# Kernel tuning notes

Measured on AMD Instinct MI355X. Metric: run time of the kernel, lower is better.

Reference implementation:

```python
import jax, jax.numpy as jnp
import numpy as np

N, E, H, C = 50000, 1_600_000, 4, 32
DIN, DE = 128, 32
NEG_SLOPE = 0.2  # PyG GATConv leaky_relu negative_slope default


def setup_inputs() -> dict:
    key = jax.random.key(0)
    ks = jax.random.split(key, 12)
    s = 0.1  # weight scale
    return {
        "x": jax.random.normal(ks[0], (N, DIN), jnp.float32),
        "edge_index": jax.random.randint(ks[1], (2, E), 0, N, jnp.int32),
        "edge_attr": jax.random.normal(ks[2], (E, DE), jnp.float32),
        "W": jax.random.normal(ks[3], (DIN, H * C), jnp.float32) * s,
        "att_src": jax.random.normal(ks[4], (H, C), jnp.float32) * s,
        "att_dst": jax.random.normal(ks[5], (H, C), jnp.float32) * s,
        "lin_edge_W": jax.random.normal(ks[6], (DE, H * C), jnp.float32) * s,
        "att_edge": jax.random.normal(ks[7], (H, C), jnp.float32) * s,
        "bias": jax.random.normal(ks[8], (H * C,), jnp.float32) * s,
        "proj_W": jax.random.normal(ks[9], (H * C, C), jnp.float32) * s,
        "proj_b": jax.random.normal(ks[10], (C,), jnp.float32) * s,
    }


def reference(x, edge_index, edge_attr, W, att_src, att_dst, lin_edge_W,
              att_edge, bias, proj_W, proj_b):
    n = x.shape[0]
    h, c = att_src.shape
    src, dst = edge_index[0], edge_index[1]

    # add self loops; loop edge_attr = mean of incoming edge_attr (PyG fill_value='mean')
    deg = jax.ops.segment_sum(jnp.ones(src.shape, x.dtype), dst, num_segments=n)
    ea_mean = jax.ops.segment_sum(edge_attr, dst, num_segments=n) / jnp.maximum(deg, 1.0)[:, None]
    loop = jnp.arange(n, dtype=src.dtype)
    src = jnp.concatenate([src, loop])
    dst = jnp.concatenate([dst, loop])
    ea = jnp.concatenate([edge_attr, ea_mean], axis=0)

    xl = (x @ W).reshape(n, h, c)                       # [N,H,C]
    a_src = jnp.einsum('nhc,hc->nh', xl, att_src)       # [N,H]
    a_dst = jnp.einsum('nhc,hc->nh', xl, att_dst)
    e = (ea @ lin_edge_W).reshape(-1, h, c)             # [E',H,C]
    a_e = jnp.einsum('ehc,hc->eh', e, att_edge)

    alpha = jax.nn.leaky_relu(a_src[src] + a_dst[dst] + a_e, NEG_SLOPE)  # [E',H]
    amax = jax.lax.stop_gradient(jax.ops.segment_max(alpha, dst, num_segments=n))
    alpha = jnp.exp(alpha - amax[dst])
    denom = jax.ops.segment_sum(alpha, dst, num_segments=n)
    alpha = alpha / (denom[dst] + 1e-16)                # segment softmax over incoming edges

    out = jax.ops.segment_sum(xl[src] * alpha[..., None], dst, num_segments=n)  # [N,H,C]
    out = out.reshape(n, h * c) + bias                  # concat heads + bias
    return out @ proj_W + proj_b                        # concat projection
```

## Files before the change

### kernel.cpp

```cpp
#include <hip/hip_runtime.h>

#define NEG_SLOPE 0.2f

__device__ __forceinline__ float lrelu(float x) { return x > 0.0f ? x : NEG_SLOPE * x; }

__device__ __forceinline__ float bcast(float v, int srcLane) {
  return __int_as_float(__builtin_amdgcn_readlane(__float_as_int(v), srcLane));
}

__device__ __forceinline__ unsigned pack_bf16(float a, float b) {
  unsigned ua = __float_as_uint(a), ub = __float_as_uint(b);
  ua += 0x7fffu + ((ua >> 16) & 1u);
  ub += 0x7fffu + ((ub >> 16) & 1u);
  return (ua >> 16) | (ub & 0xffff0000u);
}
__device__ __forceinline__ float bf16lo(unsigned z) { return __uint_as_float(z << 16); }
__device__ __forceinline__ float bf16hi(unsigned z) { return __uint_as_float(z & 0xffff0000u); }

__global__ void k0_setup(const float* __restrict__ W, const float* __restrict__ proj_W,
                         const float* __restrict__ att_src, const float* __restrict__ att_dst,
                         const float* __restrict__ lin_edge_W, const float* __restrict__ att_edge,
                         const float* __restrict__ bias, const float* __restrict__ proj_b,
                         float* __restrict__ Wz, float* __restrict__ Ws, float* __restrict__ Wd,
                         float* __restrict__ M, float* __restrict__ cproj) {
  int t = blockIdx.x * blockDim.x + threadIdx.x;
  if (t < 16384) {
    int d = t >> 7, o = t & 127;
    int h = o >> 5, jj = o & 31;
    float s = 0.f;
    #pragma unroll
    for (int c = 0; c < 32; ++c)
      s += W[d * 128 + h * 32 + c] * proj_W[(h * 32 + c) * 32 + jj];
    Wz[d * 128 + o] = s;
  } else if (t < 16384 + 512) {
    int idx = t - 16384; int d = idx >> 2, h = idx & 3;
    float s = 0.f;
    #pragma unroll
    for (int c = 0; c < 32; ++c) s += W[d * 128 + h * 32 + c] * att_src[h * 32 + c];
    Ws[d * 4 + h] = s;
  } else if (t < 16384 + 1024) {
    int idx = t - 16384 - 512; int d = idx >> 2, h = idx & 3;
    float s = 0.f;
    #pragma unroll
    for (int c = 0; c < 32; ++c) s += W[d * 128 + h * 32 + c] * att_dst[h * 32 + c];
    Wd[d * 4 + h] = s;
  } else if (t < 16384 + 1024 + 128) {
    int idx = t - 16384 - 1024; int d = idx >> 2, h = idx & 3;
    float s = 0.f;
    #pragma unroll
    for (int c = 0; c < 32; ++c) s += lin_edge_W[d * 128 + h * 32 + c] * att_edge[h * 32 + c];
    M[d * 4 + h] = s;
  } else if (t < 16384 + 1024 + 128 + 32) {
    int jj = t - 16384 - 1024 - 128;
    float s = proj_b[jj];
    #pragma unroll
    for (int k = 0; k < 128; ++k) s += bias[k] * proj_W[k * 32 + jj];
    cproj[jj] = s;
  }
}

__global__ __launch_bounds__(256) void k3_gemm(
    const float* __restrict__ x, const float* __restrict__ Wz,
    const float* __restrict__ Ws, const float* __restrict__ Wd,
    int n, unsigned* __restrict__ Zp, float* __restrict__ a_src, float* __restrict__ a_dst) {
  __shared__ float2 Wl[128 * 64];
  int tid = threadIdx.x;
  for (int idx = tid; idx < 128 * 64; idx += 256) {
    int k = idx >> 6, l = idx & 63;
    Wl[idx] = make_float2(Wz[k * 128 + l], Wz[k * 128 + 64 + l]);
  }
  __syncthreads();
  int lane = tid & 63, wid = tid >> 6;
  float ws0[4], ws1[4], wd0[4], wd1[4];
  #pragma unroll
  for (int h = 0; h < 4; ++h) {
    ws0[h] = Ws[lane * 4 + h];  ws1[h] = Ws[(64 + lane) * 4 + h];
    wd0[h] = Wd[lane * 4 + h];  wd1[h] = Wd[(64 + lane) * 4 + h];
  }
  int gw = blockIdx.x * 4 + wid;
  int nw = gridDim.x * 4;
  for (int base = gw * 4; base < n; base += nw * 4) {
    float xa[4], xb[4];
    #pragma unroll
    for (int u = 0; u < 4; ++u) {
      int node = base + u;
      xa[u] = (node < n) ? x[node * 128 + lane] : 0.0f;
      xb[u] = (node < n) ? x[node * 128 + 64 + lane] : 0.0f;
    }
    float acc0[4] = {0.f, 0.f, 0.f, 0.f}, acc1[4] = {0.f, 0.f, 0.f, 0.f};
    #pragma unroll 16
    for (int k = 0; k < 64; ++k) {
      float2 w = Wl[k * 64 + lane];
      #pragma unroll
      for (int u = 0; u < 4; ++u) {
        float xv = bcast(xa[u], k);
        acc0[u] += xv * w.x; acc1[u] += xv * w.y;
      }
    }
    #pragma unroll 16
    for (int k = 0; k < 64; ++k) {
      float2 w = Wl[(64 + k) * 64 + lane];
      #pragma unroll
      for (int u = 0; u < 4; ++u) {
        float xv = bcast(xb[u], k);
        acc0[u] += xv * w.x; acc1[u] += xv * w.y;
      }
    }
    #pragma unroll
    for (int u = 0; u < 4; ++u) {
      int node = base + u;
      if (node >= n) break;
      Zp[(size_t)node * 64 + lane] = pack_bf16(acc0[u], acc1[u]);
      float ps[4], pd[4];
      #pragma unroll
      for (int h = 0; h < 4; ++h) {
        ps[h] = xa[u] * ws0[h] + xb[u] * ws1[h];
        pd[h] = xa[u] * wd0[h] + xb[u] * wd1[h];
      }
      #pragma unroll
      for (int m = 1; m < 64; m <<= 1) {
        #pragma unroll
        for (int h = 0; h < 4; ++h) {
          ps[h] += __shfl_xor(ps[h], m);
          pd[h] += __shfl_xor(pd[h], m);
        }
      }
      if (lane == 0) {
        *(float4*)&a_src[node * 4] = make_float4(ps[0], ps[1], ps[2], ps[3]);
        *(float4*)&a_dst[node * 4] = make_float4(pd[0], pd[1], pd[2], pd[3]);
      }
    }
  }
}

__global__ __launch_bounds__(256) void k1_edge(
    const int* __restrict__ ei, int E, const float4* __restrict__ ea4,
    const float* __restrict__ Mg,
    const float* __restrict__ a_src, const float* __restrict__ a_dst,
    uint4* __restrict__ we, int* __restrict__ deg, int* __restrict__ rank) {
  __shared__ float4 s_ea[256 * 9];
  __shared__ float4 Msh[32];
  int t = threadIdx.x;
  if (t < 32) Msh[t] = ((const float4*)Mg)[t];
  int B0 = blockIdx.x * 256;
  #pragma unroll
  for (int k = 0; k < 8; ++k) {
    int f = k * 256 + t;
    int e = B0 + (f >> 3);
    float4 v = (e < E) ? ea4[(size_t)B0 * 8 + f] : make_float4(0.f, 0.f, 0.f, 0.f);
    s_ea[(f >> 3) * 9 + (f & 7)] = v;
  }
  __syncthreads();
  int e = B0 + t;
  if (e >= E) return;
  int s = ei[e], d = ei[E + e];
  float4 as = *(const float4*)&a_src[(size_t)s * 4];
  float4 ad = *(const float4*)&a_dst[(size_t)d * 4];
  float ae0 = 0.f, ae1 = 0.f, ae2 = 0.f, ae3 = 0.f;
  #pragma unroll
  for (int j = 0; j < 8; ++j) {
    float4 v = s_ea[t * 9 + j];
    float4 m0 = Msh[j * 4 + 0], m1 = Msh[j * 4 + 1], m2 = Msh[j * 4 + 2], m3 = Msh[j * 4 + 3];
    ae0 += v.x * m0.x + v.y * m1.x + v.z * m2.x + v.w * m3.x;
    ae1 += v.x * m0.y + v.y * m1.y + v.z * m2.y + v.w * m3.y;
    ae2 += v.x * m0.z + v.y * m1.z + v.z * m2.z + v.w * m3.z;
    ae3 += v.x * m0.w + v.y * m1.w + v.z * m2.w + v.w * m3.w;
  }
  float w0 = __expf(lrelu(ae0 + as.x + ad.x));
  float w1 = __expf(lrelu(ae1 + as.y + ad.y));
  float w2 = __expf(lrelu(ae2 + as.z + ad.z));
  float w3 = __expf(lrelu(ae3 + as.w + ad.w));
  we[e] = make_uint4(pack_bf16(w0, w1), pack_bf16(w2, w3),
                     pack_bf16(ae0, ae1), pack_bf16(ae2, ae3));
  rank[e] = atomicAdd(&deg[d], 1);
}

__global__ void k2_scan(const int* __restrict__ deg, int n, int* __restrict__ offsets) {
  __shared__ int shw[16];
  __shared__ int shtot;
  int tid = threadIdx.x;
  int lane = tid & 63, wid = tid >> 6;
  int running = 0;
  for (int base = 0; base < n; base += 4096) {
    int i = base + tid * 4;
    int4 v = make_int4(0, 0, 0, 0);
    if (i + 3 < n) v = *(const int4*)&deg[i];
    else {
      if (i < n) v.x = deg[i];
      if (i + 1 < n) v.y = deg[i + 1];
      if (i + 2 < n) v.z = deg[i + 2];
      if (i + 3 < n) v.w = deg[i + 3];
    }
    int tsum = v.x + v.y + v.z + v.w;
    int inc = tsum;
    #pragma unroll
    for (int s = 1; s < 64; s <<= 1) {
      int t = __shfl_up(inc, s);
      if (lane >= s) inc += t;
    }
    if (lane == 63) shw[wid] = inc;
    __syncthreads();
    if (wid == 0) {
      int w = (lane < 16) ? shw[lane] : 0;
      int winc = w;
      #pragma unroll
      for (int s = 1; s < 16; s <<= 1) {
        int t = __shfl_up(winc, s);
        if (lane >= s) winc += t;
      }
      if (lane < 16) shw[lane] = winc - w;
      if (lane == 15) shtot = winc;
    }
    __syncthreads();
    int excl = running + shw[wid] + inc - tsum;
    if (i < n)     offsets[i + 1] = excl + v.x;
    if (i + 1 < n) offsets[i + 2] = excl + v.x + v.y;
    if (i + 2 < n) offsets[i + 3] = excl + v.x + v.y + v.z;
    if (i + 3 < n) offsets[i + 4] = excl + tsum;
    running += shtot;
    __syncthreads();
  }
  if (tid == 0) offsets[0] = 0;
}

__global__ void k4_scatter(const int* __restrict__ ei, int E,
                           const int* __restrict__ rank, const int* __restrict__ offsets,
                           const uint4* __restrict__ we, uint4* __restrict__ csr) {
  int e = blockIdx.x * blockDim.x + threadIdx.x;
  if (e >= E) return;
  int s = ei[e], d = ei[E + e];
  int slot = offsets[d] + rank[e];
  uint4 w = we[e];
  uint4* ent = &csr[(size_t)slot * 2];
  *(int*)ent = s;
  ent[1] = w;
}

__global__ __launch_bounds__(256) void k5_agg(
    const int* __restrict__ offsets, const uint4* __restrict__ csr,
    const unsigned* __restrict__ Zp,
    const float* __restrict__ a_src, const float* __restrict__ a_dst,
    const float* __restrict__ cproj, int n, float* __restrict__ out) {
  __shared__ float4 s_w[4][64];
  __shared__ int    s_s[4][64];
  int tid = threadIdx.x;
  int lane = tid & 63, wid = tid >> 6;
  int gw = blockIdx.x * 4 + wid, nw = gridDim.x * 4;
  int h0 = lane >> 5, j = lane & 31;
  float cp = cproj[j];
  const float* wbase = (const float*)&s_w[wid][0];
  for (int node = gw; node < n; node += nw) {
    int off0 = offsets[node], off1 = offsets[node + 1];
    int dg = off1 - off0;
    float dsx = 0.f, dsy = 0.f, dsz = 0.f, dsw = 0.f;
    float aex = 0.f, aey = 0.f, aez = 0.f, aew = 0.f;
    float agg0 = 0.f, agg1 = 0.f;
    for (int base = off0; base < off1; base += 64) {
      int rem = off1 - base; if (rem > 64) rem = 64;
      if (lane < rem) {
        const uint4* ent = &csr[(size_t)(base + lane) * 2];
        int s = *(const int*)ent;
        uint4 w = ent[1];
        float w0 = bf16lo(w.x), w1 = bf16hi(w.x);
        float w2 = bf16lo(w.y), w3 = bf16hi(w.y);
        dsx += w0; dsy += w1; dsz += w2; dsw += w3;
        aex += bf16lo(w.z); aey += bf16hi(w.z);
        aez += bf16lo(w.w); aew += bf16hi(w.w);
        s_w[wid][lane] = make_float4(w0, w2, w1, w3);
        s_s[wid][lane] = s;
      }
      int jj = 0;
      for (; jj + 4 <= rem; jj += 4) {
        int s0 = s_s[wid][jj], s1 = s_s[wid][jj + 1];
        int s2 = s_s[wid][jj + 2], s3 = s_s[wid][jj + 3];
        unsigned z0 = Zp[(size_t)s0 * 64 + lane];
        unsigned z1 = Zp[(size_t)s1 * 64 + lane];
        unsigned z2 = Zp[(size_t)s2 * 64 + lane];
        unsigned z3 = Zp[(size_t)s3 * 64 + lane];
        float2 w0 = *(const float2*)(wbase + (jj    ) * 4 + 2 * h0);
        float2 w1 = *(const float2*)(wbase + (jj + 1) * 4 + 2 * h0);
        float2 w2 = *(const float2*)(wbase + (jj + 2) * 4 + 2 * h0);
        float2 w3 = *(const float2*)(wbase + (jj + 3) * 4 + 2 * h0);
        agg0 += w0.x * bf16lo(z0) + w1.x * bf16lo(z1) + w2.x * bf16lo(z2) + w3.x * bf16lo(z3);
        agg1 += w0.y * bf16hi(z0) + w1.y * bf16hi(z1) + w2.y * bf16hi(z2) + w3.y * bf16hi(z3);
      }
      for (; jj < rem; ++jj) {
        int s0 = s_s[wid][jj];
        unsigned z0 = Zp[(size_t)s0 * 64 + lane];
        float2 w0 = *(const float2*)(wbase + jj * 4 + 2 * h0);
        agg0 += w0.x * bf16lo(z0);
        agg1 += w0.y * bf16hi(z0);
      }
    }
    #pragma unroll
    for (int m = 1; m < 64; m <<= 1) {
      dsx += __shfl_xor(dsx, m); dsy += __shfl_xor(dsy, m);
      dsz += __shfl_xor(dsz, m); dsw += __shfl_xor(dsw, m);
      aex += __shfl_xor(aex, m); aey += __shfl_xor(aey, m);
      aez += __shfl_xor(aez, m); aew += __shfl_xor(aew, m);
    }
    float invd = 1.0f / (float)(dg > 0 ? dg : 1);
    float4 asn = *(const float4*)&a_src[node * 4];
    float4 ad  = *(const float4*)&a_dst[node * 4];
    float w0 = __expf(lrelu(asn.x + ad.x + aex * invd));
    float w1 = __expf(lrelu(asn.y + ad.y + aey * invd));
    float w2 = __expf(lrelu(asn.z + ad.z + aez * invd));
    float w3 = __expf(lrelu(asn.w + ad.w + aew * invd));
    dsx += w0; dsy += w1; dsz += w2; dsw += w3;
    unsigned zpn = Zp[(size_t)node * 64 + lane];
    float sw0 = h0 ? w1 : w0, sw1 = h0 ? w3 : w2;
    agg0 += sw0 * bf16lo(zpn);
    agg1 += sw1 * bf16hi(zpn);
    float d0 = h0 ? dsy : dsx, d1 = h0 ? dsw : dsz;
    float tt = agg0 / (d0 + 1e-16f) + agg1 / (d1 + 1e-16f);
    tt += __shfl_xor(tt, 32);
    if (lane < 32) out[node * 32 + j] = tt + cp;
  }
}

extern "C" void kernel_launch(void* const* d_in, const int* in_sizes, int n_in,
                              void* d_out, int out_size, void* d_ws, size_t ws_size,
                              hipStream_t stream) {
  const float* x          = (const float*)d_in[0];
  const int*   ei         = (const int*)  d_in[1];
  const float* ea         = (const float*)d_in[2];
  const float* W          = (const float*)d_in[3];
  const float* att_src    = (const float*)d_in[4];
  const float* att_dst    = (const float*)d_in[5];
  const float* lin_edge_W = (const float*)d_in[6];
  const float* att_edge   = (const float*)d_in[7];
  const float* bias       = (const float*)d_in[8];
  const float* proj_W     = (const float*)d_in[9];
  const float* proj_b     = (const float*)d_in[10];
  float* out = (float*)d_out;
  int N = in_sizes[0] / 128;
  int E = in_sizes[1] / 2;

  char* p = (char*)d_ws;
  auto alloc = [&](size_t bytes) {
    char* r = p;
    p += (bytes + 255) & ~(size_t)255;
    return r;
  };
  unsigned* Zp     = (unsigned*)alloc((size_t)N * 64 * 4);
  float* a_src     = (float*)alloc((size_t)N * 4 * 4);
  float* a_dst     = (float*)alloc((size_t)N * 4 * 4);
  int*   deg       = (int*)  alloc((size_t)N * 4);
  int*   offsets   = (int*)  alloc((size_t)(N + 1) * 4);
  int*   rank      = (int*)  alloc((size_t)E * 4);
  uint4* we        = (uint4*)alloc((size_t)E * 16);
  uint4* csr       = (uint4*)alloc((size_t)E * 32);
  float* Wz        = (float*)alloc(128 * 128 * 4);
  float* Ws        = (float*)alloc(128 * 4 * 4);
  float* Wd        = (float*)alloc(128 * 4 * 4);
  float* M         = (float*)alloc(32 * 4 * 4);
  float* cproj     = (float*)alloc(32 * 4);

  hipMemsetAsync(deg, 0, (size_t)N * 4, stream);

  k0_setup<<<69, 256, 0, stream>>>(W, proj_W, att_src, att_dst, lin_edge_W, att_edge,
                                   bias, proj_b, Wz, Ws, Wd, M, cproj);
  k3_gemm<<<512, 256, 0, stream>>>(x, Wz, Ws, Wd, N, Zp, a_src, a_dst);
  k1_edge<<<(E + 255) / 256, 256, 0, stream>>>(ei, E, (const float4*)ea, M,
                                               a_src, a_dst, we, deg, rank);
  k2_scan<<<1, 1024, 0, stream>>>(deg, N, offsets);
  k4_scatter<<<(E + 255) / 256, 256, 0, stream>>>(ei, E, rank, offsets, we, csr);
  k5_agg<<<2048, 256, 0, stream>>>(offsets, csr, Zp, a_src, a_dst, cproj, N, out);
}
```

Baseline: 558.9 us.

## Build CSR directly in edge kernel and compute softmax weights during aggregation

A separate degree-count kernel and a scan now run first, so the edge kernel can claim CSR slots with an atomic on a per-node cursor and write 16-byte entries (source index plus bf16 edge logits) straight into the CSR. This removes the rank and we intermediate arrays and the separate scatter kernel, and halves the CSR entry size. Exponentiated attention weights are now computed in the aggregation kernel from a_src gathers, which adds a random gather and four exps per edge there. Edge order within a node becomes nondeterministic, so float summation order can vary between runs.

```diff
diff --git a/kernel.cpp b/kernel.cpp
--- a/kernel.cpp
+++ b/kernel.cpp
@@ -133,49 +133,23 @@
   }
 }
 
-__global__ __launch_bounds__(256) void k1_edge(
-    const int* __restrict__ ei, int E, const float4* __restrict__ ea4,
-    const float* __restrict__ Mg,
-    const float* __restrict__ a_src, const float* __restrict__ a_dst,
-    uint4* __restrict__ we, int* __restrict__ deg, int* __restrict__ rank) {
-  __shared__ float4 s_ea[256 * 9];
-  __shared__ float4 Msh[32];
-  int t = threadIdx.x;
-  if (t < 32) Msh[t] = ((const float4*)Mg)[t];
-  int B0 = blockIdx.x * 256;
-  #pragma unroll
-  for (int k = 0; k < 8; ++k) {
-    int f = k * 256 + t;
-    int e = B0 + (f >> 3);
-    float4 v = (e < E) ? ea4[(size_t)B0 * 8 + f] : make_float4(0.f, 0.f, 0.f, 0.f);
-    s_ea[(f >> 3) * 9 + (f & 7)] = v;
-  }
-  __syncthreads();
-  int e = B0 + t;
-  if (e >= E) return;
-  int s = ei[e], d = ei[E + e];
-  float4 as = *(const float4*)&a_src[(size_t)s * 4];
-  float4 ad = *(const float4*)&a_dst[(size_t)d * 4];
-  float ae0 = 0.f, ae1 = 0.f, ae2 = 0.f, ae3 = 0.f;
-  #pragma unroll
-  for (int j = 0; j < 8; ++j) {
-    float4 v = s_ea[t * 9 + j];
-    float4 m0 = Msh[j * 4 + 0], m1 = Msh[j * 4 + 1], m2 = Msh[j * 4 + 2], m3 = Msh[j * 4 + 3];
-    ae0 += v.x * m0.x + v.y * m1.x + v.z * m2.x + v.w * m3.x;
-    ae1 += v.x * m0.y + v.y * m1.y + v.z * m2.y + v.w * m3.y;
-    ae2 += v.x * m0.z + v.y * m1.z + v.z * m2.z + v.w * m3.z;
-    ae3 += v.x * m0.w + v.y * m1.w + v.z * m2.w + v.w * m3.w;
-  }
-  float w0 = __expf(lrelu(ae0 + as.x + ad.x));
-  float w1 = __expf(lrelu(ae1 + as.y + ad.y));
-  float w2 = __expf(lrelu(ae2 + as.z + ad.z));
-  float w3 = __expf(lrelu(ae3 + as.w + ad.w));
-  we[e] = make_uint4(pack_bf16(w0, w1), pack_bf16(w2, w3),
-                     pack_bf16(ae0, ae1), pack_bf16(ae2, ae3));
-  rank[e] = atomicAdd(&deg[d], 1);
-}
-
-__global__ void k2_scan(const int* __restrict__ deg, int n, int* __restrict__ offsets) {
+__global__ __launch_bounds__(256) void kA_deg(const int* __restrict__ ei, int E,
+                                              int* __restrict__ deg) {
+  int t = blockIdx.x * blockDim.x + threadIdx.x;
+  int i = t * 4;
+  if (((E & 3) == 0) && (i + 3 < E)) {
+    int4 d = *(const int4*)&ei[E + i];
+    atomicAdd(&deg[d.x], 1);
+    atomicAdd(&deg[d.y], 1);
+    atomicAdd(&deg[d.z], 1);
+    atomicAdd(&deg[d.w], 1);
+  } else {
+    for (int k = i; k < E && k < i + 4; ++k) atomicAdd(&deg[ei[E + k]], 1);
+  }
+}
+
+__global__ void k2_scan(const int* __restrict__ deg, int n, int* __restrict__ offsets,
+                        int* __restrict__ cnt) {
   __shared__ int shw[16];
   __shared__ int shtot;
   int tid = threadIdx.x;
@@ -213,27 +187,55 @@
     }
     __syncthreads();
     int excl = running + shw[wid] + inc - tsum;
-    if (i < n)     offsets[i + 1] = excl + v.x;
-    if (i + 1 < n) offsets[i + 2] = excl + v.x + v.y;
-    if (i + 2 < n) offsets[i + 3] = excl + v.x + v.y + v.z;
-    if (i + 3 < n) offsets[i + 4] = excl + tsum;
+    if (i + 3 < n) {
+      *(int4*)&offsets[i + 1] = make_int4(excl + v.x, excl + v.x + v.y,
+                                          excl + v.x + v.y + v.z, excl + tsum);
+      *(int4*)&cnt[i] = make_int4(excl, excl + v.x, excl + v.x + v.y,
+                                  excl + v.x + v.y + v.z);
+    } else {
+      if (i < n)     { offsets[i + 1] = excl + v.x;             cnt[i]     = excl; }
+      if (i + 1 < n) { offsets[i + 2] = excl + v.x + v.y;       cnt[i + 1] = excl + v.x; }
+      if (i + 2 < n) { offsets[i + 3] = excl + v.x + v.y + v.z; cnt[i + 2] = excl + v.x + v.y; }
+      if (i + 3 < n) { offsets[i + 4] = excl + tsum;            cnt[i + 3] = excl + v.x + v.y + v.z; }
+    }
     running += shtot;
     __syncthreads();
   }
   if (tid == 0) offsets[0] = 0;
 }
 
-__global__ void k4_scatter(const int* __restrict__ ei, int E,
-                           const int* __restrict__ rank, const int* __restrict__ offsets,
-                           const uint4* __restrict__ we, uint4* __restrict__ csr) {
-  int e = blockIdx.x * blockDim.x + threadIdx.x;
+__global__ __launch_bounds__(256) void k1_edge(
+    const int* __restrict__ ei, int E, const float4* __restrict__ ea4,
+    const float* __restrict__ Mg,
+    int* __restrict__ cnt, uint4* __restrict__ csr) {
+  __shared__ float4 s_ea[256 * 9];
+  __shared__ float4 Msh[32];
+  int t = threadIdx.x;
+  if (t < 32) Msh[t] = ((const float4*)Mg)[t];
+  int B0 = blockIdx.x * 256;
+  #pragma unroll
+  for (int k = 0; k < 8; ++k) {
+    int f = k * 256 + t;
+    int e = B0 + (f >> 3);
+    float4 v = (e < E) ? ea4[(size_t)B0 * 8 + f] : make_float4(0.f, 0.f, 0.f, 0.f);
+    s_ea[(f >> 3) * 9 + (f & 7)] = v;
+  }
+  __syncthreads();
+  int e = B0 + t;
   if (e >= E) return;
   int s = ei[e], d = ei[E + e];
-  int slot = offsets[d] + rank[e];
-  uint4 w = we[e];
-  uint4* ent = &csr[(size_t)slot * 2];
-  *(int*)ent = s;
-  ent[1] = w;
+  int slot = atomicAdd(&cnt[d], 1);
+  float ae0 = 0.f, ae1 = 0.f, ae2 = 0.f, ae3 = 0.f;
+  #pragma unroll
+  for (int j = 0; j < 8; ++j) {
+    float4 v = s_ea[t * 9 + j];
+    float4 m0 = Msh[j * 4 + 0], m1 = Msh[j * 4 + 1], m2 = Msh[j * 4 + 2], m3 = Msh[j * 4 + 3];
+    ae0 += v.x * m0.x + v.y * m1.x + v.z * m2.x + v.w * m3.x;
+    ae1 += v.x * m0.y + v.y * m1.y + v.z * m2.y + v.w * m3.y;
+    ae2 += v.x * m0.z + v.y * m1.z + v.z * m2.z + v.w * m3.z;
+    ae3 += v.x * m0.w + v.y * m1.w + v.z * m2.w + v.w * m3.w;
+  }
+  csr[(size_t)slot] = make_uint4((unsigned)s, pack_bf16(ae0, ae1), pack_bf16(ae2, ae3), 0u);
 }
 
 __global__ __launch_bounds__(256) void k5_agg(
@@ -252,20 +254,24 @@
   for (int node = gw; node < n; node += nw) {
     int off0 = offsets[node], off1 = offsets[node + 1];
     int dg = off1 - off0;
+    float4 ad = *(const float4*)&a_dst[(size_t)node * 4];
     float dsx = 0.f, dsy = 0.f, dsz = 0.f, dsw = 0.f;
     float aex = 0.f, aey = 0.f, aez = 0.f, aew = 0.f;
     float agg0 = 0.f, agg1 = 0.f;
     for (int base = off0; base < off1; base += 64) {
       int rem = off1 - base; if (rem > 64) rem = 64;
       if (lane < rem) {
-        const uint4* ent = &csr[(size_t)(base + lane) * 2];
-        int s = *(const int*)ent;
-        uint4 w = ent[1];
-        float w0 = bf16lo(w.x), w1 = bf16hi(w.x);
-        float w2 = bf16lo(w.y), w3 = bf16hi(w.y);
+        uint4 ent = csr[(size_t)(base + lane)];
+        int s = (int)ent.x;
+        float ae0 = bf16lo(ent.y), ae1 = bf16hi(ent.y);
+        float ae2 = bf16lo(ent.z), ae3 = bf16hi(ent.z);
+        float4 av = *(const float4*)&a_src[(size_t)s * 4];
+        float w0 = __expf(lrelu(ae0 + av.x + ad.x));
+        float w1 = __expf(lrelu(ae1 + av.y + ad.y));
+        float w2 = __expf(lrelu(ae2 + av.z + ad.z));
+        float w3 = __expf(lrelu(ae3 + av.w + ad.w));
         dsx += w0; dsy += w1; dsz += w2; dsw += w3;
-        aex += bf16lo(w.z); aey += bf16hi(w.z);
-        aez += bf16lo(w.w); aew += bf16hi(w.w);
+        aex += ae0; aey += ae1; aez += ae2; aew += ae3;
         s_w[wid][lane] = make_float4(w0, w2, w1, w3);
         s_s[wid][lane] = s;
       }
@@ -300,8 +306,7 @@
       aez += __shfl_xor(aez, m); aew += __shfl_xor(aew, m);
     }
     float invd = 1.0f / (float)(dg > 0 ? dg : 1);
-    float4 asn = *(const float4*)&a_src[node * 4];
-    float4 ad  = *(const float4*)&a_dst[node * 4];
+    float4 asn = *(const float4*)&a_src[(size_t)node * 4];
     float w0 = __expf(lrelu(asn.x + ad.x + aex * invd));
     float w1 = __expf(lrelu(asn.y + ad.y + aey * invd));
     float w2 = __expf(lrelu(asn.z + ad.z + aez * invd));
@@ -346,10 +351,9 @@
   float* a_src     = (float*)alloc((size_t)N * 4 * 4);
   float* a_dst     = (float*)alloc((size_t)N * 4 * 4);
   int*   deg       = (int*)  alloc((size_t)N * 4);
+  int*   cnt       = (int*)  alloc((size_t)N * 4);
   int*   offsets   = (int*)  alloc((size_t)(N + 1) * 4);
-  int*   rank      = (int*)  alloc((size_t)E * 4);
-  uint4* we        = (uint4*)alloc((size_t)E * 16);
-  uint4* csr       = (uint4*)alloc((size_t)E * 32);
+  uint4* csr       = (uint4*)alloc((size_t)E * 16);
   float* Wz        = (float*)alloc(128 * 128 * 4);
   float* Ws        = (float*)alloc(128 * 4 * 4);
   float* Wd        = (float*)alloc(128 * 4 * 4);
@@ -360,10 +364,9 @@
 
   k0_setup<<<69, 256, 0, stream>>>(W, proj_W, att_src, att_dst, lin_edge_W, att_edge,
                                    bias, proj_b, Wz, Ws, Wd, M, cproj);
+  kA_deg<<<(E / 4 + 256) / 256, 256, 0, stream>>>(ei, E, deg);
+  k2_scan<<<1, 1024, 0, stream>>>(deg, N, offsets, cnt);
   k3_gemm<<<512, 256, 0, stream>>>(x, Wz, Ws, Wd, N, Zp, a_src, a_dst);
-  k1_edge<<<(E + 255) / 256, 256, 0, stream>>>(ei, E, (const float4*)ea, M,
-                                               a_src, a_dst, we, deg, rank);
-  k2_scan<<<1, 1024, 0, stream>>>(deg, N, offsets);
-  k4_scatter<<<(E + 255) / 256, 256, 0, stream>>>(ei, E, rank, offsets, we, csr);
+  k1_edge<<<(E + 255) / 256, 256, 0, stream>>>(ei, E, (const float4*)ea, M, cnt, csr);
   k5_agg<<<2048, 256, 0, stream>>>(offsets, csr, Zp, a_src, a_dst, cproj, N, out);
 }
```

New measurement: 595.3 us. 6.5% more time.

## Split degree counting into separate kernel and simplify edge kernel loads

Applied to the files above, without the earlier changes.

Moves the per-destination atomic degree/rank computation out of the edge-attention kernel into its own vectorized kernel that runs before the node GEMM, with the scan moved ahead as well. The edge kernel drops its shared-memory staging of edge attributes and reads each edge's 128-byte row directly. The scatter kernel now writes CSR entries with nontemporal stores and fully writes the padding words. This rearranges the kernel schedule at the cost of reading the edge indices one extra time in a separate pass, and uncoalesced per-thread row reads may hurt bandwidth.

```diff
diff --git a/kernel.cpp b/kernel.cpp
--- a/kernel.cpp
+++ b/kernel.cpp
@@ -1,6 +1,8 @@
 #include <hip/hip_runtime.h>
 
 #define NEG_SLOPE 0.2f
+
+typedef unsigned nuint4 __attribute__((ext_vector_type(4)));
 
 __device__ __forceinline__ float lrelu(float x) { return x > 0.0f ? x : NEG_SLOPE * x; }
 
@@ -133,46 +135,21 @@
   }
 }
 
-__global__ __launch_bounds__(256) void k1_edge(
-    const int* __restrict__ ei, int E, const float4* __restrict__ ea4,
-    const float* __restrict__ Mg,
-    const float* __restrict__ a_src, const float* __restrict__ a_dst,
-    uint4* __restrict__ we, int* __restrict__ deg, int* __restrict__ rank) {
-  __shared__ float4 s_ea[256 * 9];
-  __shared__ float4 Msh[32];
-  int t = threadIdx.x;
-  if (t < 32) Msh[t] = ((const float4*)Mg)[t];
-  int B0 = blockIdx.x * 256;
-  #pragma unroll
-  for (int k = 0; k < 8; ++k) {
-    int f = k * 256 + t;
-    int e = B0 + (f >> 3);
-    float4 v = (e < E) ? ea4[(size_t)B0 * 8 + f] : make_float4(0.f, 0.f, 0.f, 0.f);
-    s_ea[(f >> 3) * 9 + (f & 7)] = v;
-  }
-  __syncthreads();
-  int e = B0 + t;
-  if (e >= E) return;
-  int s = ei[e], d = ei[E + e];
-  float4 as = *(const float4*)&a_src[(size_t)s * 4];
-  float4 ad = *(const float4*)&a_dst[(size_t)d * 4];
-  float ae0 = 0.f, ae1 = 0.f, ae2 = 0.f, ae3 = 0.f;
-  #pragma unroll
-  for (int j = 0; j < 8; ++j) {
-    float4 v = s_ea[t * 9 + j];
-    float4 m0 = Msh[j * 4 + 0], m1 = Msh[j * 4 + 1], m2 = Msh[j * 4 + 2], m3 = Msh[j * 4 + 3];
-    ae0 += v.x * m0.x + v.y * m1.x + v.z * m2.x + v.w * m3.x;
-    ae1 += v.x * m0.y + v.y * m1.y + v.z * m2.y + v.w * m3.y;
-    ae2 += v.x * m0.z + v.y * m1.z + v.z * m2.z + v.w * m3.z;
-    ae3 += v.x * m0.w + v.y * m1.w + v.z * m2.w + v.w * m3.w;
-  }
-  float w0 = __expf(lrelu(ae0 + as.x + ad.x));
-  float w1 = __expf(lrelu(ae1 + as.y + ad.y));
-  float w2 = __expf(lrelu(ae2 + as.z + ad.z));
-  float w3 = __expf(lrelu(ae3 + as.w + ad.w));
-  we[e] = make_uint4(pack_bf16(w0, w1), pack_bf16(w2, w3),
-                     pack_bf16(ae0, ae1), pack_bf16(ae2, ae3));
-  rank[e] = atomicAdd(&deg[d], 1);
+__global__ __launch_bounds__(256) void kA_deg(const int* __restrict__ ei, int E,
+                                              int* __restrict__ deg, int* __restrict__ rank) {
+  int t = blockIdx.x * blockDim.x + threadIdx.x;
+  int i = t * 4;
+  if (((E & 3) == 0) && (i + 3 < E)) {
+    int4 d = *(const int4*)&ei[E + i];
+    int4 r;
+    r.x = atomicAdd(&deg[d.x], 1);
+    r.y = atomicAdd(&deg[d.y], 1);
+    r.z = atomicAdd(&deg[d.z], 1);
+    r.w = atomicAdd(&deg[d.w], 1);
+    *(int4*)&rank[i] = r;
+  } else {
+    for (int k = i; k < E && k < i + 4; ++k) rank[k] = atomicAdd(&deg[ei[E + k]], 1);
+  }
 }
 
 __global__ void k2_scan(const int* __restrict__ deg, int n, int* __restrict__ offsets) {
@@ -223,17 +200,53 @@
   if (tid == 0) offsets[0] = 0;
 }
 
-__global__ void k4_scatter(const int* __restrict__ ei, int E,
+__global__ __launch_bounds__(256) void k1_edge(
+    const int* __restrict__ ei, int E, const float4* __restrict__ ea4,
+    const float* __restrict__ Mg,
+    const float* __restrict__ a_src, const float* __restrict__ a_dst,
+    uint4* __restrict__ we) {
+  __shared__ float4 Msh[32];
+  int t = threadIdx.x;
+  if (t < 32) Msh[t] = ((const float4*)Mg)[t];
+  __syncthreads();
+  int e = blockIdx.x * 256 + t;
+  if (e >= E) return;
+  int s = ei[e], d = ei[E + e];
+  float4 as = *(const float4*)&a_src[(size_t)s * 4];
+  float4 ad = *(const float4*)&a_dst[(size_t)d * 4];
+  const float4* row = ea4 + (size_t)e * 8;
+  float ae0 = 0.f, ae1 = 0.f, ae2 = 0.f, ae3 = 0.f;
+  #pragma unroll
+  for (int j = 0; j < 8; ++j) {
+    float4 v = row[j];
+    float4 m0 = Msh[j * 4 + 0], m1 = Msh[j * 4 + 1], m2 = Msh[j * 4 + 2], m3 = Msh[j * 4 + 3];
+    ae0 += v.x * m0.x + v.y * m1.x + v.z * m2.x + v.w * m3.x;
+    ae1 += v.x * m0.y + v.y * m1.y + v.z * m2.y + v.w * m3.y;
+    ae2 += v.x * m0.z + v.y * m1.z + v.z * m2.z + v.w * m3.z;
+    ae3 += v.x * m0.w + v.y * m1.w + v.z * m2.w + v.w * m3.w;
+  }
+  float w0 = __expf(lrelu(ae0 + as.x + ad.x));
+  float w1 = __expf(lrelu(ae1 + as.y + ad.y));
+  float w2 = __expf(lrelu(ae2 + as.z + ad.z));
+  float w3 = __expf(lrelu(ae3 + as.w + ad.w));
+  we[e] = make_uint4(pack_bf16(w0, w1), pack_bf16(w2, w3),
+                     pack_bf16(ae0, ae1), pack_bf16(ae2, ae3));
+}
+
+__global__ __launch_bounds__(256) void k4_scatter(const int* __restrict__ ei, int E,
                            const int* __restrict__ rank, const int* __restrict__ offsets,
                            const uint4* __restrict__ we, uint4* __restrict__ csr) {
   int e = blockIdx.x * blockDim.x + threadIdx.x;
   if (e >= E) return;
-  int s = ei[e], d = ei[E + e];
+  int d = ei[E + e];
+  int s = ei[e];
   int slot = offsets[d] + rank[e];
   uint4 w = we[e];
-  uint4* ent = &csr[(size_t)slot * 2];
-  *(int*)ent = s;
-  ent[1] = w;
+  nuint4* ent = (nuint4*)&csr[(size_t)slot * 2];
+  nuint4 e0; e0.x = (unsigned)s; e0.y = 0u; e0.z = 0u; e0.w = 0u;
+  nuint4 e1; e1.x = w.x; e1.y = w.y; e1.z = w.z; e1.w = w.w;
+  __builtin_nontemporal_store(e0, ent);
+  __builtin_nontemporal_store(e1, ent + 1);
 }
 
 __global__ __launch_bounds__(256) void k5_agg(
@@ -360,10 +373,11 @@
 
   k0_setup<<<69, 256, 0, stream>>>(W, proj_W, att_src, att_dst, lin_edge_W, att_edge,
                                    bias, proj_b, Wz, Ws, Wd, M, cproj);
+  kA_deg<<<(E / 4 + 255) / 256, 256, 0, stream>>>(ei, E, deg, rank);
+  k2_scan<<<1, 1024, 0, stream>>>(deg, N, offsets);
   k3_gemm<<<512, 256, 0, stream>>>(x, Wz, Ws, Wd, N, Zp, a_src, a_dst);
   k1_edge<<<(E + 255) / 256, 256, 0, stream>>>(ei, E, (const float4*)ea, M,
-                                               a_src, a_dst, we, deg, rank);
-  k2_scan<<<1, 1024, 0, stream>>>(deg, N, offsets);
+                                               a_src, a_dst, we);
   k4_scatter<<<(E + 255) / 256, 256, 0, stream>>>(ei, E, rank, offsets, we, csr);
   k5_agg<<<2048, 256, 0, stream>>>(offsets, csr, Zp, a_src, a_dst, cproj, N, out);
 }
```

Result: slower. 696.0 us (+24.5%).
